# Performance work log

Hardware: AMD Instinct MI355X
Metric: run time of the kernel (lower is better)

Reference implementation:

```python
import jax, jax.numpy as jnp
import numpy as np

B = 512; S = 6; Q = 2            # meta-batch, n_way*k_shot, n_way*q_query
DIM = 64; IMG = 28; N_WAY = 2
HEADS = 4; HD = DIM // HEADS     # retrieval heads / head dim
EPS = 1e-5


def _pool_mat(inp, out):
    # exact torch AdaptiveAvgPool2d windowing as a matrix [out, inp]
    P = np.zeros((out, inp), np.float32)
    for i in range(out):
        s = (i * inp) // out
        e = -((-(i + 1) * inp) // out)
        P[i, s:e] = 1.0 / (e - s)
    return jnp.asarray(P)

P28 = _pool_mat(IMG, 8)  # 28 -> 8; subsequent 8 -> 8 pools are identity


def _gelu(x):
    return jax.nn.gelu(x, approximate=False)


def _conv(x, w, b):
    y = jax.lax.conv_general_dilated(x, w, (1, 1), ((1, 1), (1, 1)),
                                     dimension_numbers=('NCHW', 'OIHW', 'NCHW'))
    return y + b[None, :, None, None]


def _bn(x, p):
    # p rows: gamma, beta, running_mean, running_var (eval-mode BatchNorm2d)
    g, bt, m, v = p[0], p[1], p[2], p[3]
    sc = g / jnp.sqrt(v + EPS)
    return (x - m[None, :, None, None]) * sc[None, :, None, None] + bt[None, :, None, None]


def _img_in(x, c1w, c1b, bn1, c2w, c2b, bn2, c3w, c3b, bn3, c4w, c4b, bn4, lin_w):
    h = _bn(_conv(x, c1w, c1b), bn1)
    h = jnp.einsum('oi,ncij,pj->ncop', P28, h, P28)   # adaptive avg pool 28x28 -> 8x8
    h = _gelu(h)                                       # dropout is identity in eval
    h = _gelu(_bn(_conv(h, c2w, c2b), bn2))
    h = _gelu(_bn(_conv(h, c3w, c3b), bn3))
    h = _gelu(_bn(_conv(h, c4w, c4b), bn4))            # -> [N,1,8,8]
    h = h.reshape(h.shape[0], -1)                      # [N,64]
    return h @ lin_w.T                                 # Linear(64 -> DIM, no bias)


def _net(x, w1, w2):
    # x: [B,K,D]; w1,w2: [B,D,D] batched fast weights
    h = jnp.einsum('bed,bkd->bke', w1, x)
    ah = _gelu(h)
    y = jnp.einsum('bed,bkd->bke', w2, ah)
    return y, h


def _get_lor(x, w1, w2, r_q, r_k, r_v, r_o, ln_w, ln_b):
    b, k, _ = x.shape
    q, _ = _net(x, w1, w2)
    qh = jnp.einsum('nhd,bkd->bknh', r_q, q)
    sc = jnp.einsum('bknh,rnh->bknr', qh, r_k) / (HD ** 0.5)
    p = jax.nn.softmax(sc, axis=-1)
    lor = jnp.einsum('bknr,rnh->bknh', p, r_v).reshape(b, k, DIM)
    lor = jnp.einsum('de,bkd->bke', r_o, lor)
    z = lor + x
    mu = z.mean(-1, keepdims=True)
    var = ((z - mu) ** 2).mean(-1, keepdims=True)
    return (z - mu) / jnp.sqrt(var + EPS) * ln_w + ln_b


def _forward(query_w, sxs, qxs, inner_lr, c1w, c1b, bn1, c2w, c2b, bn2, c3w, c3b, bn3,
             c4w, c4b, bn4, lin_w, emb, w1, w2, tags, r_q, r_k, r_v, r_o, ln_w, ln_b,
             sys, qys):
    b = query_w.shape[0]
    s = sxs.shape[1]
    q = qxs.shape[1]
    feats = lambda im: _img_in(im.reshape(-1, 1, IMG, IMG), c1w, c1b, bn1, c2w, c2b,
                               bn2, c3w, c3b, bn3, c4w, c4b, bn4, lin_w)
    sx = feats(sxs).reshape(b, s, DIM)
    qx = feats(qxs).reshape(b, q, DIM)
    qe = tags[4]
    w1b = jnp.broadcast_to(w1, (b, DIM, DIM))
    w2b = jnp.broadcast_to(w2, (b, DIM, DIM))
    bound = sx + emb[sys]                                          # [B,S,D]
    # all 4 tag variants for all S shots in one vectorized get_lor call
    inp = (bound[:, :, None, :] + tags[:4][None, None]).reshape(b, s * 4, DIM)
    lors = _get_lor(inp, w1b, w2b, r_q, r_k, r_v, r_o, ln_w, ln_b).reshape(b, s, 4, DIM)
    l1s, r1s, l2s, r2s = lors[:, :, 0], lors[:, :, 1], lors[:, :, 2], lors[:, :, 3]
    qw1 = w1[None] + jnp.einsum('bsl,bsr->blr', l1s, r1s)
    qw2 = w2[None] + jnp.einsum('bsl,bsr->blr', l2s, r2s)
    preds, _ = _net(qx + qe, qw1, qw2)                             # [B,Q,D]
    logits = jnp.einsum('ld,bqd->bql', emb, preds).reshape(-1, N_WAY)
    labels = qys.reshape(-1)
    ls = jax.nn.log_softmax(logits)
    task_loss = -jnp.take_along_axis(ls, labels[:, None], axis=1).mean()
    n_correct = (jnp.argmax(logits, axis=1) == labels).sum()
    return task_loss, n_correct, b * q


def setup_inputs() -> dict:
    key = jax.random.key(0)
    ks = jax.random.split(key, 24)
    rn = lambda i, sh, sc=1.0: sc * jax.random.normal(ks[i], sh, jnp.float32)
    def bnp(i, c):
        k0, k1, k2 = jax.random.split(ks[i], 3)
        return jnp.stack([1.0 + 0.1 * jax.random.normal(k0, (c,)),
                          0.1 * jax.random.normal(k1, (c,)),
                          0.1 * jax.random.normal(k2, (c,)),
                          0.5 + jax.random.uniform(jax.random.fold_in(ks[i], 3), (c,))])
    return {
        'query_w': rn(0, (B, DIM)),
        'sxs': rn(1, (B, S, IMG * IMG)),
        'qxs': rn(2, (B, Q, IMG * IMG)),
        'inner_lr': jnp.float32(0.1),
        'c1w': rn(3, (32, 1, 3, 3), 0.3), 'c1b': rn(4, (32,), 0.1), 'bn1': bnp(5, 32),
        'c2w': rn(6, (32, 32, 3, 3), 0.06), 'c2b': rn(7, (32,), 0.1), 'bn2': bnp(8, 32),
        'c3w': rn(9, (32, 32, 3, 3), 0.06), 'c3b': rn(10, (32,), 0.1), 'bn3': bnp(11, 32),
        'c4w': rn(12, (1, 32, 3, 3), 0.06), 'c4b': rn(13, (1,), 0.1), 'bn4': bnp(14, 1),
        'lin_w': rn(15, (DIM, 64), 0.125),
        'emb': rn(16, (N_WAY, DIM), 0.125),
        'w1': rn(17, (DIM, DIM), 0.125),
        'w2': rn(18, (DIM, DIM), 0.125),
        'tags': rn(19, (8, DIM), 0.125),
        'r_q': rn(20, (HEADS, HD, DIM), 0.125),
        'r_k': rn(21, (16, HEADS, HD), 0.25),
        'r_v': rn(22, (16, HEADS, HD), 0.25),
        'r_o': rn(23, (DIM, DIM), 0.125),
        'ln_w': 0.001 * jnp.ones((DIM,), jnp.float32),
        'ln_b': jnp.zeros((DIM,), jnp.float32),
        'sys': jax.random.randint(jax.random.fold_in(key, 100), (B, S), 0, N_WAY),
        'qys': jax.random.randint(jax.random.fold_in(key, 101), (B, Q), 0, N_WAY),
    }


def reference(query_w, sxs, qxs, inner_lr, c1w, c1b, bn1, c2w, c2b, bn2, c3w, c3b, bn3,
              c4w, c4b, bn4, lin_w, emb, w1, w2, tags, r_q, r_k, r_v, r_o, ln_w, ln_b,
              sys, qys):
    task_loss, n_correct, n_q = _forward(query_w, sxs, qxs, inner_lr, c1w, c1b, bn1,
                                         c2w, c2b, bn2, c3w, c3b, bn3, c4w, c4b, bn4,
                                         lin_w, emb, w1, w2, tags, r_q, r_k, r_v, r_o,
                                         ln_w, ln_b, sys, qys)
    return (task_loss, task_loss, jnp.float32(0.0), n_correct, n_q)
```

## Files before the change

### kernel.cpp

```cpp
#include <hip/hip_runtime.h>
#include <math.h>

constexpr int NSUP = 3072;
constexpr float EPSF = 1e-5f;

constexpr int WS_W1B  = 0;
constexpr int WS_B1   = 1024;
constexpr int WS_W2B  = 1056;
constexpr int WS_W3B  = 5664;
constexpr int WS_W4B  = 10272;
constexpr int WS_B4   = 10416;
constexpr int WS_B2   = 10420;
constexpr int WS_B3   = 10452;
constexpr int WS_HW1  = 10484;
constexpr int WS_HW2  = 12788;
constexpr int WS_HRQ  = 15092;
constexpr int WS_HROT = 17396;
constexpr int WS_ACC  = 19700;
constexpr int WS_FEATS= 20724;

using short8 = __attribute__((ext_vector_type(8))) short;
using f32x4  = __attribute__((ext_vector_type(4))) float;

__device__ __forceinline__ float gelu_f(float x) {
    float u = 0.79788456080286535588f * x * (1.0f + 0.044715f * x * x);
    return x * __fdividef(1.0f, 1.0f + __expf(-2.0f * u));
}
__device__ __forceinline__ unsigned short f2bf(float f) {
    unsigned u = __float_as_uint(f);
    return (unsigned short)((u + 0x7FFFu + ((u >> 16) & 1u)) >> 16);
}
__device__ __forceinline__ float bflo(unsigned u) { return __uint_as_float(u << 16); }
__device__ __forceinline__ float bfhi(unsigned u) { return __uint_as_float(u & 0xffff0000u); }

__global__ void __launch_bounds__(256) precompute_kernel(
    const float* __restrict__ c1w, const float* __restrict__ c1b, const float* __restrict__ bn1,
    const float* __restrict__ c2w, const float* __restrict__ c2b, const float* __restrict__ bn2,
    const float* __restrict__ c3w, const float* __restrict__ c3b, const float* __restrict__ bn3,
    const float* __restrict__ c4w, const float* __restrict__ c4b, const float* __restrict__ bn4,
    const float* __restrict__ w1, const float* __restrict__ w2,
    const float* __restrict__ rq, const float* __restrict__ ro,
    float* __restrict__ ws)
{
    const int gid = blockIdx.x * 256 + threadIdx.x;
    const int gsz = gridDim.x * 256;

    if (gid < 4) ws[WS_ACC + gid] = 0.f;

    unsigned short* w1b = (unsigned short*)(ws + WS_W1B);
    for (int v = gid; v < 2048; v += gsz) {
        int kt = v >> 10, rem = v & 1023, oc = rem >> 5, kk = rem & 31;
        int tap = kt * 32 + kk;
        unsigned short o = 0;
        if (tap < 36) {
            int tt = tap / 6, s = tap - tt * 6;
            float sum = 0.f;
            for (int di = 0; di < 3; ++di) {
                int a = tt - di; if (a < 0 || a > 3) continue;
                for (int dj = 0; dj < 3; ++dj) {
                    int bb = s - dj; if (bb < 0 || bb > 3) continue;
                    sum += c1w[oc * 9 + di * 3 + dj];
                }
            }
            float sc1 = bn1[oc] * rsqrtf(bn1[96 + oc] + EPSF);
            o = f2bf(sum * sc1 * (1.0f / 16.0f));
        }
        w1b[v] = o;
    }
    for (int c = gid; c < 32; c += gsz) {
        float sc1 = bn1[c] * rsqrtf(bn1[96 + c] + EPSF);
        ws[WS_B1 + c] = (c1b[c] - bn1[64 + c]) * sc1 + bn1[32 + c];
        float sc2 = bn2[c] * rsqrtf(bn2[96 + c] + EPSF);
        ws[WS_B2 + c] = (c2b[c] - bn2[64 + c]) * sc2 + bn2[32 + c];
        float sc3 = bn3[c] * rsqrtf(bn3[96 + c] + EPSF);
        ws[WS_B3 + c] = (c3b[c] - bn3[64 + c]) * sc3 + bn3[32 + c];
    }
    unsigned short* w2b = (unsigned short*)(ws + WS_W2B);
    unsigned short* w3b = (unsigned short*)(ws + WS_W3B);
    for (int v = gid; v < 9216; v += gsz) {
        int tap = v >> 10, oc = (v >> 5) & 31, ic = v & 31;
        float sc2 = bn2[oc] * rsqrtf(bn2[96 + oc] + EPSF);
        float sc3 = bn3[oc] * rsqrtf(bn3[96 + oc] + EPSF);
        w2b[v] = f2bf(c2w[oc * 288 + ic * 9 + tap] * sc2);
        w3b[v] = f2bf(c3w[oc * 288 + ic * 9 + tap] * sc3);
    }
    {
        unsigned short* w4b = (unsigned short*)(ws + WS_W4B);
        float sc4 = bn4[0] * rsqrtf(bn4[3] + EPSF);
        for (int v = gid; v < 288; v += gsz) {
            int tap = v >> 5, ic = v & 31;
            w4b[v] = f2bf(c4w[ic * 9 + tap] * sc4);
        }
        if (gid == 0) ws[WS_B4] = (c4b[0] - bn4[2]) * sc4 + bn4[1];
    }
    unsigned short* hw1 = (unsigned short*)(ws + WS_HW1);
    unsigned short* hw2 = (unsigned short*)(ws + WS_HW2);
    unsigned short* hrq = (unsigned short*)(ws + WS_HRQ);
    unsigned short* hro = (unsigned short*)(ws + WS_HROT);
    for (int v = gid; v < 4608; v += gsz) {
        int e = v / 72, d = v - e * 72;
        unsigned short a = 0, b = 0, c = 0, r = 0;
        if (d < 64) {
            a = f2bf(w1[e * 64 + d]);
            b = f2bf(w2[e * 64 + d]);
            c = f2bf(rq[e * 64 + d]);
            r = f2bf(ro[d * 64 + e]);
        }
        hw1[v] = a; hw2[v] = b; hrq[v] = c; hro[v] = r;
    }
}

__global__ void __launch_bounds__(128, 6) feats_kernel(
    const float* __restrict__ sxs, const float* __restrict__ qxs,
    const float* __restrict__ lin_w, const float* __restrict__ ws,
    float* __restrict__ feats)
{
    __shared__ __align__(16) unsigned short sAct[2][3200];
    __shared__ __align__(16) float sh4[2][64];

    const int t    = threadIdx.x;
    const int wv   = t >> 6;
    const int lane = t & 63;
    const int col  = lane & 15;
    const int quad = lane >> 4;
    const int n    = blockIdx.x * 2 + wv;

    unsigned short* A = sAct[wv];

    {
        uint4 z = {0, 0, 0, 0};
        for (int i = lane; i < 400; i += 64) ((uint4*)A)[i] = z;
    }

    {
        const unsigned short* w1b = (const unsigned short*)(ws + WS_W1B);
        const float* img = (n < NSUP) ? (sxs + (size_t)n * 784) : (qxs + (size_t)(n - NSUP) * 784);
        int ttj[8], ssj[8];
        #pragma unroll
        for (int j = 0; j < 8; ++j) {
            int k = quad * 8 + j;
            ttj[j] = k / 6; ssj[j] = k - ttj[j] * 6;
        }
        f32x4 acc[4][2];
        #pragma unroll
        for (int mt = 0; mt < 4; ++mt) { acc[mt][0] = (f32x4){0,0,0,0}; acc[mt][1] = (f32x4){0,0,0,0}; }

        short8 b00 = *(const short8*)(w1b + (0 * 16 + col) * 32 + quad * 8);
        short8 b01 = *(const short8*)(w1b + (1 * 16 + col) * 32 + quad * 8);
        short8 b10 = *(const short8*)(w1b + 1024 + (0 * 16 + col) * 32 + quad * 8);
        short8 b11 = *(const short8*)(w1b + 1024 + (1 * 16 + col) * 32 + quad * 8);

        #pragma unroll
        for (int mt = 0; mt < 4; ++mt) {
            int px = mt * 16 + col;
            int sr = (((px >> 3) * 7) >> 1) - 1;
            int sc = (((px & 7) * 7) >> 1) - 1;
            short8 a0;
            #pragma unroll
            for (int j = 0; j < 8; ++j) {
                int rr = sr + ttj[j], cc = sc + ssj[j];
                float v = ((unsigned)rr < 28u && (unsigned)cc < 28u) ? img[rr * 28 + cc] : 0.f;
                a0[j] = (short)f2bf(v);
            }
            acc[mt][0] = __builtin_amdgcn_mfma_f32_16x16x32_bf16(a0, b00, acc[mt][0], 0, 0, 0);
            acc[mt][1] = __builtin_amdgcn_mfma_f32_16x16x32_bf16(a0, b01, acc[mt][1], 0, 0, 0);
            short8 a1 = {0,0,0,0,0,0,0,0};
            if (quad == 0) {
                #pragma unroll
                for (int j = 0; j < 4; ++j) {
                    int rr = sr + 5, cc = sc + 2 + j;
                    float v = ((unsigned)rr < 28u && (unsigned)cc < 28u) ? img[rr * 28 + cc] : 0.f;
                    a1[j] = (short)f2bf(v);
                }
            }
            acc[mt][0] = __builtin_amdgcn_mfma_f32_16x16x32_bf16(a1, b10, acc[mt][0], 0, 0, 0);
            acc[mt][1] = __builtin_amdgcn_mfma_f32_16x16x32_bf16(a1, b11, acc[mt][1], 0, 0, 0);
        }
        float bi0 = ws[WS_B1 + col], bi1 = ws[WS_B1 + 16 + col];
        #pragma unroll
        for (int mt = 0; mt < 4; ++mt)
            #pragma unroll
            for (int reg = 0; reg < 4; ++reg) {
                int px = mt * 16 + quad * 4 + reg;
                unsigned short* dst = A + (((px >> 3) + 1) * 10 + (px & 7) + 1) * 32;
                dst[col]      = f2bf(gelu_f(acc[mt][0][reg] + bi0));
                dst[col + 16] = f2bf(gelu_f(acc[mt][1][reg] + bi1));
            }
    }

    #pragma unroll 1
    for (int layer = 0; layer < 2; ++layer) {
        const unsigned short* wb = (const unsigned short*)(ws + (layer ? WS_W3B : WS_W2B));
        f32x4 acc[4][2];
        #pragma unroll
        for (int mt = 0; mt < 4; ++mt) { acc[mt][0] = (f32x4){0,0,0,0}; acc[mt][1] = (f32x4){0,0,0,0}; }
        const unsigned short* abase[4];
        #pragma unroll
        for (int mt = 0; mt < 4; ++mt) {
            int px = mt * 16 + col;
            abase[mt] = A + ((px >> 3) * 10 + (px & 7)) * 32 + quad * 8;
        }
        #pragma unroll
        for (int dr = 0; dr < 3; ++dr)
            #pragma unroll
            for (int dc = 0; dc < 3; ++dc) {
                int tap = dr * 3 + dc;
                short8 b0 = *(const short8*)(wb + (tap * 32 + col) * 32 + quad * 8);
                short8 b1 = *(const short8*)(wb + (tap * 32 + 16 + col) * 32 + quad * 8);
                #pragma unroll
                for (int mt = 0; mt < 4; ++mt) {
                    short8 a = *(const short8*)(abase[mt] + (dr * 10 + dc) * 32);
                    acc[mt][0] = __builtin_amdgcn_mfma_f32_16x16x32_bf16(a, b0, acc[mt][0], 0, 0, 0);
                    acc[mt][1] = __builtin_amdgcn_mfma_f32_16x16x32_bf16(a, b1, acc[mt][1], 0, 0, 0);
                }
            }
        float bi0 = ws[(layer ? WS_B3 : WS_B2) + col];
        float bi1 = ws[(layer ? WS_B3 : WS_B2) + 16 + col];
        #pragma unroll
        for (int mt = 0; mt < 4; ++mt)
            #pragma unroll
            for (int reg = 0; reg < 4; ++reg) {
                int px = mt * 16 + quad * 4 + reg;
                unsigned short* dst = A + (((px >> 3) + 1) * 10 + (px & 7) + 1) * 32;
                dst[col]      = f2bf(gelu_f(acc[mt][0][reg] + bi0));
                dst[col + 16] = f2bf(gelu_f(acc[mt][1][reg] + bi1));
            }
    }

    {
        f32x4 acc4[4];
        #pragma unroll
        for (int mt = 0; mt < 4; ++mt) acc4[mt] = (f32x4){0,0,0,0};
        const unsigned short* abase[4];
        #pragma unroll
        for (int mt = 0; mt < 4; ++mt) {
            int px = mt * 16 + col;
            abase[mt] = A + ((px >> 3) * 10 + (px & 7)) * 32 + quad * 8;
        }
        const unsigned short* w4g = (const unsigned short*)(ws + WS_W4B);
        #pragma unroll
        for (int dr = 0; dr < 3; ++dr)
            #pragma unroll
            for (int dc = 0; dc < 3; ++dc) {
                int tap = dr * 3 + dc;
                short8 b = *(const short8*)(w4g + tap * 32 + quad * 8);
                #pragma unroll
                for (int mt = 0; mt < 4; ++mt) {
                    short8 a = *(const short8*)(abase[mt] + (dr * 10 + dc) * 32);
                    acc4[mt] = __builtin_amdgcn_mfma_f32_16x16x32_bf16(a, b, acc4[mt], 0, 0, 0);
                }
            }
        if (col < 4) {
            f32x4 v = acc4[0];
            if (col == 1) v = acc4[1];
            else if (col == 2) v = acc4[2];
            else if (col == 3) v = acc4[3];
            float b4 = ws[WS_B4];
            #pragma unroll
            for (int reg = 0; reg < 4; ++reg)
                sh4[wv][col * 16 + quad * 4 + reg] = gelu_f(v[reg] + b4);
        }
    }

    {
        const float4* lw = (const float4*)(lin_w + (size_t)lane * 64);
        const float4* hp = (const float4*)sh4[wv];
        float acc = 0.f;
        #pragma unroll
        for (int j = 0; j < 16; ++j) {
            float4 w = lw[j], h = hp[j];
            acc += w.x * h.x + w.y * h.y + w.z * h.z + w.w * h.w;
        }
        feats[n * 64 + lane] = acc;
    }
}

__device__ __forceinline__ void head_gemm(const unsigned short* __restrict__ Ab,
                                          const unsigned short* __restrict__ Bw,
                                          int col, int quad, int wvid, f32x4 res[2])
{
    #pragma unroll
    for (int u = 0; u < 2; ++u) {
        int tau = wvid + u * 4;
        int mt = tau & 1, nt = tau >> 1;
        f32x4 acc = {0, 0, 0, 0};
        #pragma unroll
        for (int kt = 0; kt < 2; ++kt) {
            short8 a = *(const short8*)(Ab + (mt * 16 + col) * 72 + kt * 32 + quad * 8);
            short8 b = *(const short8*)(Bw + (nt * 16 + col) * 72 + kt * 32 + quad * 8);
            acc = __builtin_amdgcn_mfma_f32_16x16x32_bf16(a, b, acc, 0, 0, 0);
        }
        res[u] = acc;
    }
}

__global__ void __launch_bounds__(256, 4) head_kernel(
    const float* __restrict__ emb, const float* __restrict__ tags,
    const float* __restrict__ rk, const float* __restrict__ rv,
    const float* __restrict__ lnw, const float* __restrict__ lnb,
    const int* __restrict__ sys, const int* __restrict__ qys,
    const float* __restrict__ ws, const float* __restrict__ feats,
    float* __restrict__ acc_ws, float* __restrict__ out)
{
    __shared__ __align__(16) unsigned short bufA[2304], bufB[2304];
    __shared__ __align__(16) float sXf[1536];
    __shared__ __align__(16) float s_xq[128], s_ah[128], s_yp[128];
    __shared__ float s_t1[12], s_t2[12], s_mu[24], s_rs[24], s_lg[4];

    const int t    = threadIdx.x;
    const int b    = blockIdx.x;
    const int wvid = t >> 6;
    const int col  = t & 15;
    const int quad = (t >> 4) & 3;

    const unsigned short* W1g = (const unsigned short*)(ws + WS_HW1);
    const unsigned short* W2g = (const unsigned short*)(ws + WS_HW2);
    const unsigned short* RQg = (const unsigned short*)(ws + WS_HRQ);
    const unsigned short* ROg = (const unsigned short*)(ws + WS_HROT);

    if (t < 72) {
        uint4 z = {0, 0, 0, 0};
        ((uint4*)(bufA + 1728))[t] = z;
        ((uint4*)(bufB + 1728))[t] = z;
    }
    for (int idx = t; idx < 1536; idx += 256) {
        int k = idx >> 6, e = idx & 63;
        int s = k >> 2, tg = k & 3;
        int cls = sys[b * 6 + s];
        float v = feats[(b * 6 + s) * 64 + e] + emb[cls * 64 + e] + tags[tg * 64 + e];
        sXf[idx] = v;
        bufA[k * 72 + e] = f2bf(v);
    }
    __syncthreads();

    f32x4 r[2];
    head_gemm(bufA, W1g, col, quad, wvid, r);
    #pragma unroll
    for (int u = 0; u < 2; ++u) {
        int tau = wvid + u * 4, mt = tau & 1, nt = tau >> 1;
        #pragma unroll
        for (int reg = 0; reg < 4; ++reg) {
            int row = mt * 16 + quad * 4 + reg;
            if (row < 24) bufB[row * 72 + nt * 16 + col] = f2bf(gelu_f(r[u][reg]));
        }
    }
    __syncthreads();
    head_gemm(bufB, W2g, col, quad, wvid, r);
    #pragma unroll
    for (int u = 0; u < 2; ++u) {
        int tau = wvid + u * 4, mt = tau & 1, nt = tau >> 1;
        #pragma unroll
        for (int reg = 0; reg < 4; ++reg) {
            int row = mt * 16 + quad * 4 + reg;
            if (row < 24) bufA[row * 72 + nt * 16 + col] = f2bf(r[u][reg]);
        }
    }
    __syncthreads();
    head_gemm(bufA, RQg, col, quad, wvid, r);
    #pragma unroll
    for (int u = 0; u < 2; ++u) {
        int tau = wvid + u * 4, mt = tau & 1, nt = tau >> 1;
        #pragma unroll
        for (int reg = 0; reg < 4; ++reg) {
            int row = mt * 16 + quad * 4 + reg;
            if (row < 24) bufB[row * 72 + nt * 16 + col] = f2bf(r[u][reg]);
        }
    }
    __syncthreads();

    if (t < 96) {
        int k = t >> 2, nn = t & 3;
        const unsigned short* qp = bufB + k * 72 + nn * 16;
        uint4 u0 = *(const uint4*)(qp);
        uint4 u1 = *(const uint4*)(qp + 8);
        float qv[16];
        qv[0]=bflo(u0.x); qv[1]=bfhi(u0.x); qv[2]=bflo(u0.y); qv[3]=bfhi(u0.y);
        qv[4]=bflo(u0.z); qv[5]=bfhi(u0.z); qv[6]=bflo(u0.w); qv[7]=bfhi(u0.w);
        qv[8]=bflo(u1.x); qv[9]=bfhi(u1.x); qv[10]=bflo(u1.y); qv[11]=bfhi(u1.y);
        qv[12]=bflo(u1.z); qv[13]=bfhi(u1.z); qv[14]=bflo(u1.w); qv[15]=bfhi(u1.w);
        float sc[16]; float mx = -1e30f;
        #pragma unroll
        for (int rr = 0; rr < 16; ++rr) {
            const float* kp = rk + rr * 64 + nn * 16;
            float d = 0.f;
            #pragma unroll
            for (int h = 0; h < 16; ++h) d += qv[h] * kp[h];
            d *= 0.25f;
            sc[rr] = d; mx = fmaxf(mx, d);
        }
        float sum = 0.f;
        #pragma unroll
        for (int rr = 0; rr < 16; ++rr) { sc[rr] = expf(sc[rr] - mx); sum += sc[rr]; }
        float inv = 1.0f / sum;
        float o[16];
        #pragma unroll
        for (int h = 0; h < 16; ++h) o[h] = 0.f;
        #pragma unroll
        for (int rr = 0; rr < 16; ++rr) {
            const float* vp = rv + rr * 64 + nn * 16;
            float p = sc[rr];
            #pragma unroll
            for (int h = 0; h < 16; ++h) o[h] += p * vp[h];
        }
        unsigned short* op = bufA + k * 72 + nn * 16;
        #pragma unroll
        for (int h = 0; h < 16; ++h) op[h] = f2bf(o[h] * inv);
    }
    __syncthreads();

    head_gemm(bufA, ROg, col, quad, wvid, r);
    #pragma unroll
    for (int u = 0; u < 2; ++u) {
        int tau = wvid + u * 4, mt = tau & 1, nt = tau >> 1;
        #pragma unroll
        for (int reg = 0; reg < 4; ++reg) {
            int row = mt * 16 + quad * 4 + reg;
            if (row < 24) {
                int idx = row * 64 + nt * 16 + col;
                sXf[idx] = sXf[idx] + r[u][reg];
            }
        }
    }
    __syncthreads();

    if (t < 24) {
        const float4* zp = (const float4*)(sXf + t * 64);
        float sx_ = 0.f;
        #pragma unroll
        for (int j = 0; j < 16; ++j) {
            float4 v = zp[(j + t) & 15];
            sx_ += v.x + v.y + v.z + v.w;
        }
        float mu = sx_ * (1.0f / 64.0f);
        float vv = 0.f;
        #pragma unroll
        for (int j = 0; j < 16; ++j) {
            float4 v = zp[(j + t) & 15];
            float d0 = v.x - mu, d1 = v.y - mu, d2 = v.z - mu, d3 = v.w - mu;
            vv += d0*d0 + d1*d1 + d2*d2 + d3*d3;
        }
        s_mu[t] = mu;
        s_rs[t] = 1.0f / sqrtf(vv * (1.0f / 64.0f) + EPSF);
    }
    __syncthreads();
    for (int idx = t; idx < 1536; idx += 256) {
        int k = idx >> 6, e = idx & 63;
        float v = (sXf[idx] - s_mu[k]) * s_rs[k] * lnw[e] + lnb[e];
        bufB[k * 72 + e] = f2bf(v);
    }
    if (t < 128) {
        int q = t >> 6, e = t & 63;
        s_xq[t] = feats[(NSUP + b * 2 + q) * 64 + e] + tags[256 + e];
    }
    __syncthreads();

    if (t < 12) {
        int q = t / 6, s = t - q * 6;
        const uint4* rp = (const uint4*)(bufB + (s * 4 + 1) * 72);
        const float* xp = s_xq + q * 64;
        float d = 0.f;
        #pragma unroll
        for (int j = 0; j < 8; ++j) {
            uint4 u = rp[j];
            const float* x = xp + j * 8;
            d += bflo(u.x)*x[0] + bfhi(u.x)*x[1] + bflo(u.y)*x[2] + bfhi(u.y)*x[3]
               + bflo(u.z)*x[4] + bfhi(u.z)*x[5] + bflo(u.w)*x[6] + bfhi(u.w)*x[7];
        }
        s_t1[t] = d;
    }
    __syncthreads();
    if (t < 128) {
        int q = t >> 6, e = t & 63;
        const uint4* wp = (const uint4*)(W1g + e * 72);
        const float* xp = s_xq + q * 64;
        float acc = 0.f;
        #pragma unroll
        for (int j = 0; j < 8; ++j) {
            uint4 u = wp[j];
            const float* x = xp + j * 8;
            acc += bflo(u.x)*x[0] + bfhi(u.x)*x[1] + bflo(u.y)*x[2] + bfhi(u.y)*x[3]
                 + bflo(u.z)*x[4] + bfhi(u.z)*x[5] + bflo(u.w)*x[6] + bfhi(u.w)*x[7];
        }
        #pragma unroll
        for (int s = 0; s < 6; ++s)
            acc += bflo((unsigned)bufB[(s * 4 + 0) * 72 + e]) * s_t1[q * 6 + s];
        s_ah[t] = gelu_f(acc);
    }
    __syncthreads();
    if (t < 12) {
        int q = t / 6, s = t - q * 6;
        const uint4* rp = (const uint4*)(bufB + (s * 4 + 3) * 72);
        const float* xp = s_ah + q * 64;
        float d = 0.f;
        #pragma unroll
        for (int j = 0; j < 8; ++j) {
            uint4 u = rp[j];
            const float* x = xp + j * 8;
            d += bflo(u.x)*x[0] + bfhi(u.x)*x[1] + bflo(u.y)*x[2] + bfhi(u.y)*x[3]
               + bflo(u.z)*x[4] + bfhi(u.z)*x[5] + bflo(u.w)*x[6] + bfhi(u.w)*x[7];
        }
        s_t2[t] = d;
    }
    __syncthreads();
    if (t < 128) {
        int q = t >> 6, e = t & 63;
        const uint4* wp = (const uint4*)(W2g + e * 72);
        const float* xp = s_ah + q * 64;
        float acc = 0.f;
        #pragma unroll
        for (int j = 0; j < 8; ++j) {
            uint4 u = wp[j];
            const float* x = xp + j * 8;
            acc += bflo(u.x)*x[0] + bfhi(u.x)*x[1] + bflo(u.y)*x[2] + bfhi(u.y)*x[3]
                 + bflo(u.z)*x[4] + bfhi(u.z)*x[5] + bflo(u.w)*x[6] + bfhi(u.w)*x[7];
        }
        #pragma unroll
        for (int s = 0; s < 6; ++s)
            acc += bflo((unsigned)bufB[(s * 4 + 2) * 72 + e]) * s_t2[q * 6 + s];
        s_yp[t] = acc;
    }
    __syncthreads();
    if (t < 4) {
        int q = t >> 1, ll = t & 1;
        const float4* ep = (const float4*)(emb + ll * 64);
        const float4* yp = (const float4*)(s_yp + q * 64);
        float d = 0.f;
        #pragma unroll
        for (int j = 0; j < 16; ++j) {
            float4 a = ep[j], x = yp[j];
            d += a.x*x.x + a.y*x.y + a.z*x.z + a.w*x.w;
        }
        s_lg[t] = d;
    }
    __syncthreads();
    if (t == 0) {
        float lsum = 0.f, corr = 0.f;
        #pragma unroll
        for (int q = 0; q < 2; ++q) {
            float l0 = s_lg[q * 2], l1 = s_lg[q * 2 + 1];
            int lab = qys[b * 2 + q];
            float m = fmaxf(l0, l1);
            float lse = m + logf(expf(l0 - m) + expf(l1 - m));
            lsum += -((lab ? l1 : l0) - lse);
            int pred = (l1 > l0) ? 1 : 0;
            corr += (pred == lab) ? 1.0f : 0.0f;
        }
        atomicAdd(acc_ws + 0, lsum);
        atomicAdd(acc_ws + 1, corr);
        __threadfence();
        unsigned old = atomicAdd((unsigned*)(acc_ws + 2), 1u);
        if (old == 511u) {
            float tot_l = atomicAdd(acc_ws + 0, 0.f);
            float tot_c = atomicAdd(acc_ws + 1, 0.f);
            float loss = tot_l * (1.0f / 1024.0f);
            out[0] = loss;
            out[1] = loss;
            out[2] = 0.0f;
            out[3] = tot_c;
            out[4] = 1024.0f;
        }
    }
}

extern "C" void kernel_launch(void* const* d_in, const int* in_sizes, int n_in,
                              void* d_out, int out_size, void* d_ws, size_t ws_size,
                              hipStream_t stream)
{
    (void)in_sizes; (void)n_in; (void)out_size; (void)ws_size;
    const float* sxs  = (const float*)d_in[1];
    const float* qxs  = (const float*)d_in[2];
    const float* c1w  = (const float*)d_in[4];
    const float* c1b  = (const float*)d_in[5];
    const float* bn1  = (const float*)d_in[6];
    const float* c2w  = (const float*)d_in[7];
    const float* c2b  = (const float*)d_in[8];
    const float* bn2  = (const float*)d_in[9];
    const float* c3w  = (const float*)d_in[10];
    const float* c3b  = (const float*)d_in[11];
    const float* bn3  = (const float*)d_in[12];
    const float* c4w  = (const float*)d_in[13];
    const float* c4b  = (const float*)d_in[14];
    const float* bn4  = (const float*)d_in[15];
    const float* lin_w= (const float*)d_in[16];
    const float* emb  = (const float*)d_in[17];
    const float* w1   = (const float*)d_in[18];
    const float* w2   = (const float*)d_in[19];
    const float* tags = (const float*)d_in[20];
    const float* rq   = (const float*)d_in[21];
    const float* rk   = (const float*)d_in[22];
    const float* rv   = (const float*)d_in[23];
    const float* ro   = (const float*)d_in[24];
    const float* lnw  = (const float*)d_in[25];
    const float* lnb  = (const float*)d_in[26];
    const int*   sys  = (const int*)d_in[27];
    const int*   qys  = (const int*)d_in[28];

    float* ws  = (float*)d_ws;
    float* out = (float*)d_out;

    precompute_kernel<<<64, 256, 0, stream>>>(c1w, c1b, bn1, c2w, c2b, bn2,
                                              c3w, c3b, bn3, c4w, c4b, bn4,
                                              w1, w2, rq, ro, ws);
    feats_kernel<<<2048, 128, 0, stream>>>(sxs, qxs, lin_w, ws, ws + WS_FEATS);
    head_kernel<<<512, 256, 0, stream>>>(emb, tags, rk, rv, lnw, lnb, sys, qys,
                                         ws, ws + WS_FEATS, ws + WS_ACC, out);
}
```

Baseline: 199.2 us.

## Split each image's conv tower across two waves sharing one LDS buffer

```diff
diff --git a/kernel.cpp b/kernel.cpp
--- a/kernel.cpp
+++ b/kernel.cpp
@@ -110,27 +110,28 @@
     }
 }
 
-__global__ void __launch_bounds__(128, 6) feats_kernel(
+__global__ void __launch_bounds__(128, 8) feats_kernel(
     const float* __restrict__ sxs, const float* __restrict__ qxs,
     const float* __restrict__ lin_w, const float* __restrict__ ws,
     float* __restrict__ feats)
 {
-    __shared__ __align__(16) unsigned short sAct[2][3200];
-    __shared__ __align__(16) float sh4[2][64];
+    __shared__ __align__(16) unsigned short sAct[3200];
+    __shared__ __align__(16) float sh4[64];
 
     const int t    = threadIdx.x;
     const int wv   = t >> 6;
     const int lane = t & 63;
     const int col  = lane & 15;
     const int quad = lane >> 4;
-    const int n    = blockIdx.x * 2 + wv;
-
-    unsigned short* A = sAct[wv];
+    const int n    = blockIdx.x;
+
+    unsigned short* A = sAct;
 
     {
         uint4 z = {0, 0, 0, 0};
-        for (int i = lane; i < 400; i += 64) ((uint4*)A)[i] = z;
-    }
+        for (int i = t; i < 400; i += 128) ((uint4*)A)[i] = z;
+    }
+    __syncthreads();
 
     {
         const unsigned short* w1b = (const unsigned short*)(ws + WS_W1B);
@@ -141,9 +142,9 @@
             int k = quad * 8 + j;
             ttj[j] = k / 6; ssj[j] = k - ttj[j] * 6;
         }
-        f32x4 acc[4][2];
-        #pragma unroll
-        for (int mt = 0; mt < 4; ++mt) { acc[mt][0] = (f32x4){0,0,0,0}; acc[mt][1] = (f32x4){0,0,0,0}; }
+        f32x4 acc[2][2];
+        #pragma unroll
+        for (int mt = 0; mt < 2; ++mt) { acc[mt][0] = (f32x4){0,0,0,0}; acc[mt][1] = (f32x4){0,0,0,0}; }
 
         short8 b00 = *(const short8*)(w1b + (0 * 16 + col) * 32 + quad * 8);
         short8 b01 = *(const short8*)(w1b + (1 * 16 + col) * 32 + quad * 8);
@@ -151,8 +152,8 @@
         short8 b11 = *(const short8*)(w1b + 1024 + (1 * 16 + col) * 32 + quad * 8);
 
         #pragma unroll
-        for (int mt = 0; mt < 4; ++mt) {
-            int px = mt * 16 + col;
+        for (int mt = 0; mt < 2; ++mt) {
+            int px = wv * 32 + mt * 16 + col;
             int sr = (((px >> 3) * 7) >> 1) - 1;
             int sc = (((px & 7) * 7) >> 1) - 1;
             short8 a0;
@@ -178,26 +179,27 @@
         }
         float bi0 = ws[WS_B1 + col], bi1 = ws[WS_B1 + 16 + col];
         #pragma unroll
-        for (int mt = 0; mt < 4; ++mt)
+        for (int mt = 0; mt < 2; ++mt)
             #pragma unroll
             for (int reg = 0; reg < 4; ++reg) {
-                int px = mt * 16 + quad * 4 + reg;
+                int px = wv * 32 + mt * 16 + quad * 4 + reg;
                 unsigned short* dst = A + (((px >> 3) + 1) * 10 + (px & 7) + 1) * 32;
                 dst[col]      = f2bf(gelu_f(acc[mt][0][reg] + bi0));
                 dst[col + 16] = f2bf(gelu_f(acc[mt][1][reg] + bi1));
             }
     }
+    __syncthreads();
 
     #pragma unroll 1
     for (int layer = 0; layer < 2; ++layer) {
         const unsigned short* wb = (const unsigned short*)(ws + (layer ? WS_W3B : WS_W2B));
-        f32x4 acc[4][2];
-        #pragma unroll
-        for (int mt = 0; mt < 4; ++mt) { acc[mt][0] = (f32x4){0,0,0,0}; acc[mt][1] = (f32x4){0,0,0,0}; }
-        const unsigned short* abase[4];
-        #pragma unroll
-        for (int mt = 0; mt < 4; ++mt) {
-            int px = mt * 16 + col;
+        f32x4 acc[2][2];
+        #pragma unroll
+        for (int mt = 0; mt < 2; ++mt) { acc[mt][0] = (f32x4){0,0,0,0}; acc[mt][1] = (f32x4){0,0,0,0}; }
+        const unsigned short* abase[2];
+        #pragma unroll
+        for (int mt = 0; mt < 2; ++mt) {
+            int px = wv * 32 + mt * 16 + col;
             abase[mt] = A + ((px >> 3) * 10 + (px & 7)) * 32 + quad * 8;
         }
         #pragma unroll
@@ -208,33 +210,34 @@
                 short8 b0 = *(const short8*)(wb + (tap * 32 + col) * 32 + quad * 8);
                 short8 b1 = *(const short8*)(wb + (tap * 32 + 16 + col) * 32 + quad * 8);
                 #pragma unroll
-                for (int mt = 0; mt < 4; ++mt) {
+                for (int mt = 0; mt < 2; ++mt) {
                     short8 a = *(const short8*)(abase[mt] + (dr * 10 + dc) * 32);
                     acc[mt][0] = __builtin_amdgcn_mfma_f32_16x16x32_bf16(a, b0, acc[mt][0], 0, 0, 0);
                     acc[mt][1] = __builtin_amdgcn_mfma_f32_16x16x32_bf16(a, b1, acc[mt][1], 0, 0, 0);
                 }
             }
+        __syncthreads();
         float bi0 = ws[(layer ? WS_B3 : WS_B2) + col];
         float bi1 = ws[(layer ? WS_B3 : WS_B2) + 16 + col];
         #pragma unroll
-        for (int mt = 0; mt < 4; ++mt)
+        for (int mt = 0; mt < 2; ++mt)
             #pragma unroll
             for (int reg = 0; reg < 4; ++reg) {
-                int px = mt * 16 + quad * 4 + reg;
+                int px = wv * 32 + mt * 16 + quad * 4 + reg;
                 unsigned short* dst = A + (((px >> 3) + 1) * 10 + (px & 7) + 1) * 32;
                 dst[col]      = f2bf(gelu_f(acc[mt][0][reg] + bi0));
                 dst[col + 16] = f2bf(gelu_f(acc[mt][1][reg] + bi1));
             }
+        __syncthreads();
     }
 
     {
-        f32x4 acc4[4];
-        #pragma unroll
-        for (int mt = 0; mt < 4; ++mt) acc4[mt] = (f32x4){0,0,0,0};
-        const unsigned short* abase[4];
-        #pragma unroll
-        for (int mt = 0; mt < 4; ++mt) {
-            int px = mt * 16 + col;
+        f32x4 acc4[2];
+        acc4[0] = (f32x4){0,0,0,0}; acc4[1] = (f32x4){0,0,0,0};
+        const unsigned short* abase[2];
+        #pragma unroll
+        for (int mt = 0; mt < 2; ++mt) {
+            int px = wv * 32 + mt * 16 + col;
             abase[mt] = A + ((px >> 3) * 10 + (px & 7)) * 32 + quad * 8;
         }
         const unsigned short* w4g = (const unsigned short*)(ws + WS_W4B);
@@ -245,33 +248,31 @@
                 int tap = dr * 3 + dc;
                 short8 b = *(const short8*)(w4g + tap * 32 + quad * 8);
                 #pragma unroll
-                for (int mt = 0; mt < 4; ++mt) {
+                for (int mt = 0; mt < 2; ++mt) {
                     short8 a = *(const short8*)(abase[mt] + (dr * 10 + dc) * 32);
                     acc4[mt] = __builtin_amdgcn_mfma_f32_16x16x32_bf16(a, b, acc4[mt], 0, 0, 0);
                 }
             }
-        if (col < 4) {
-            f32x4 v = acc4[0];
-            if (col == 1) v = acc4[1];
-            else if (col == 2) v = acc4[2];
-            else if (col == 3) v = acc4[3];
+        if (col < 2) {
+            f32x4 v = (col == 0) ? acc4[0] : acc4[1];
             float b4 = ws[WS_B4];
             #pragma unroll
             for (int reg = 0; reg < 4; ++reg)
-                sh4[wv][col * 16 + quad * 4 + reg] = gelu_f(v[reg] + b4);
-        }
-    }
-
-    {
-        const float4* lw = (const float4*)(lin_w + (size_t)lane * 64);
-        const float4* hp = (const float4*)sh4[wv];
+                sh4[wv * 32 + col * 16 + quad * 4 + reg] = gelu_f(v[reg] + b4);
+        }
+    }
+    __syncthreads();
+
+    if (t < 64) {
+        const float4* lw = (const float4*)(lin_w + (size_t)t * 64);
+        const float4* hp = (const float4*)sh4;
         float acc = 0.f;
         #pragma unroll
         for (int j = 0; j < 16; ++j) {
             float4 w = lw[j], h = hp[j];
             acc += w.x * h.x + w.y * h.y + w.z * h.z + w.w * h.w;
         }
-        feats[n * 64 + lane] = acc;
+        feats[n * 64 + t] = acc;
     }
 }
 
@@ -601,7 +602,7 @@
     precompute_kernel<<<64, 256, 0, stream>>>(c1w, c1b, bn1, c2w, c2b, bn2,
                                               c3w, c3b, bn3, c4w, c4b, bn4,
                                               w1, w2, rq, ro, ws);
-    feats_kernel<<<2048, 128, 0, stream>>>(sxs, qxs, lin_w, ws, ws + WS_FEATS);
+    feats_kernel<<<4096, 128, 0, stream>>>(sxs, qxs, lin_w, ws, ws + WS_FEATS);
     head_kernel<<<512, 256, 0, stream>>>(emb, tags, rk, rv, lnw, lnb, sys, qys,
                                          ws, ws + WS_FEATS, ws + WS_ACC, out);
 }
```

Measured after the change: 195.3 us. No clear change (-1.9%).
